# Kernel optimization log

Measured on AMD Instinct MI355X. Metric: run time of the kernel, lower is better.

Reference implementation:

```python
import jax, jax.numpy as jnp
import numpy as np

B, C, H, W = 4, 128, 128, 128
G, K = 4, 3
P = K * K
STRIDE, PAD, DIL = 1, 1, 1
OFFSET_SCALE = 1.0


def setup_inputs() -> dict:
    key = jax.random.key(0)
    k1, k2, k3, k4 = jax.random.split(key, 4)
    inp = jax.random.normal(k1, (B, C, H, W), jnp.float32)
    # offset / mask linear params (zero-init in source; small random here for a
    # nontrivial sampling pattern -- same math, different param values)
    W_off = jax.random.normal(k2, (C, G * P * 2), jnp.float32) * 0.01
    b_off = jax.random.normal(k3, (G * P * 2,), jnp.float32) * 0.5
    W_mask = jax.random.normal(k4, (C, G * P), jnp.float32) * 0.02
    b_mask = jnp.zeros((G * P,), jnp.float32)
    return {"inp": inp, "W_off": W_off, "b_off": b_off, "W_mask": W_mask, "b_mask": b_mask}


def _dcnv3_core(x, offset, mask):
    # x: (b,h,w,c)  offset: (b,h,w,G*P*2)  mask: (b,h,w,G*P)
    b, h, w, c = x.shape
    gc = c // G
    xp = jnp.pad(x, ((0, 0), (PAD, PAD), (PAD, PAD), (0, 0)))
    H_in, W_in = h + 2 * PAD, w + 2 * PAD
    H_out = (H_in - (DIL * (K - 1) + 1)) // STRIDE + 1
    W_out = (W_in - (DIL * (K - 1) + 1)) // STRIDE + 1
    Q = H_out * W_out

    # reference points, normalized to padded size (matches _get_reference_points)
    base = (DIL * (K - 1)) // 2 + 0.5
    ref_y = (base + jnp.arange(H_out, dtype=jnp.float32) * STRIDE) / H_in
    ref_x = (base + jnp.arange(W_out, dtype=jnp.float32) * STRIDE) / W_in
    ref = jnp.stack(jnp.broadcast_arrays(ref_x[None, :], ref_y[:, None]), -1)  # (Ho,Wo,2) as (x,y)

    # dilation grid (matches _generate_dilation_grids; torch meshgrid flatten is x-major)
    off0 = -((DIL * (K - 1)) // 2)
    ks = off0 + jnp.arange(K, dtype=jnp.float32) * DIL
    gx = jnp.repeat(ks, K) / W_in  # (P,)
    gy = jnp.tile(ks, K) / H_in
    grid = jnp.stack([gx, gy], -1)  # (P,2), identical for every group

    norm = jnp.array([W_in, H_in], jnp.float32)
    loc = (ref[None, :, :, None, None, :]
           + grid[None, None, None, None, :, :] * OFFSET_SCALE
           + offset.reshape(b, H_out, W_out, G, P, 2) * (OFFSET_SCALE / norm))  # (b,Ho,Wo,G,P,2)

    # grid_sample(bilinear, zeros, align_corners=False): pixel = loc*size - 0.5
    px = loc[..., 0] * W_in - 0.5
    py = loc[..., 1] * H_in - 0.5
    x0 = jnp.floor(px); y0 = jnp.floor(py)
    tx = px - x0; ty = py - y0
    x0i = x0.astype(jnp.int32); y0i = y0.astype(jnp.int32)

    xg = xp.reshape(b, H_in * W_in, G, gc)

    def corner(ix, iy, wgt):
        valid = (ix >= 0) & (ix < W_in) & (iy >= 0) & (iy < H_in)
        lin = jnp.clip(iy, 0, H_in - 1) * W_in + jnp.clip(ix, 0, W_in - 1)
        idx = lin.reshape(b, Q, G, P).transpose(0, 1, 3, 2).reshape(b, Q * P, G)
        g = jnp.take_along_axis(xg, idx[..., None], axis=1)  # (b,Q*P,G,gc)
        wv = jnp.where(valid, wgt, 0.0).reshape(b, Q, G, P).transpose(0, 1, 3, 2).reshape(b, Q * P, G, 1)
        return g * wv

    val = (corner(x0i, y0i, (1 - tx) * (1 - ty))
           + corner(x0i + 1, y0i, tx * (1 - ty))
           + corner(x0i, y0i + 1, (1 - tx) * ty)
           + corner(x0i + 1, y0i + 1, tx * ty))  # (b,Q*P,G,gc)

    m = mask.reshape(b, Q, G, P).transpose(0, 1, 3, 2).reshape(b, Q, P, G, 1)
    out = (val.reshape(b, Q, P, G, gc) * m).sum(axis=2)  # (b,Q,G,gc)
    return out.reshape(b, H_out, W_out, G * gc)


def reference(inp, W_off, b_off, W_mask, b_mask):
    b, c, h, w = inp.shape
    x = inp.reshape(b, h, w, c)  # torch .view reinterpretation (faithful to source)
    offset = x @ W_off + b_off  # (b,h,w,G*P*2)
    mask = jax.nn.softmax((x @ W_mask + b_mask).reshape(b, h, w, G, P), axis=-1).reshape(b, h, w, G * P)
    out = _dcnv3_core(x, offset, mask)  # (b,h,w,c)
    return out.reshape(b, c, h, w)
```

## Files before the change

kernel.cpp:

```cpp
#include <hip/hip_runtime.h>


#define NPIX 65536

typedef unsigned int uint;
typedef unsigned short ushort;
typedef __attribute__((ext_vector_type(8))) short short8v;
typedef __attribute__((ext_vector_type(4))) float f32x4;

__device__ __forceinline__ ushort f2bf(float f) {
  uint u = __float_as_uint(f);
  u += 0x7FFFu + ((u >> 16) & 1u);
  return (ushort)(u >> 16);
}
__device__ __forceinline__ uint pkbf(float lo, float hi) {
  return (uint)f2bf(lo) | ((uint)f2bf(hi) << 16);
}
__device__ __forceinline__ float bflo(uint d) { return __uint_as_float(d << 16); }
__device__ __forceinline__ float bfhi(uint d) { return __uint_as_float(d & 0xFFFF0000u); }

union U8 { uint u[4]; short8v v; };

__global__ __launch_bounds__(256) void dcn_lin_mfma(
    const float* __restrict__ x, const float* __restrict__ Woff,
    const float* __restrict__ boff, const float* __restrict__ Wmask,
    const float* __restrict__ bmask, float* __restrict__ ws,
    ushort* __restrict__ x16) {
  __shared__ uint wt[112 * 68];
  __shared__ float bias_lds[112];
  const int pbase = blockIdx.x << 6;
  const int t = threadIdx.x;

  {
    int n = t, row = 0;
    bool act = true;
    if (t >= 224) act = false;
    else if (t >= 112) { n = t - 112; row = 1; }
    if (act) {
      for (int kp = row; kp < 64; kp += 2) {
        const int k = kp << 1;
        float w0, w1;
        if (n < 72) {
          w0 = Woff[k * 72 + n];        w1 = Woff[k * 72 + 72 + n];
        } else if (n < 108) {
          w0 = Wmask[k * 36 + n - 72];  w1 = Wmask[k * 36 + 36 + n - 72];
        } else {
          w0 = 0.f; w1 = 0.f;
        }
        wt[n * 68 + kp] = pkbf(w0, w1);
      }
    }
    if (t < 112)
      bias_lds[t] = (t < 72) ? boff[t] : (t < 108 ? bmask[t - 72] : 0.f);
  }

  if (x16) {
    const int pix2 = pbase + (t >> 2);
    const int quad = t & 3;
    const float* xp = x + (size_t)pix2 * 128 + (quad << 5);
    const int bb = pix2 >> 14, yx = pix2 & 16383;
    ushort* dst = x16 + ((((size_t)((quad << 2) | bb) << 14) | yx) << 5);
#pragma unroll
    for (int ck = 0; ck < 2; ++ck) {
      const float4 a = *(const float4*)(xp + ck * 16);
      const float4 b4 = *(const float4*)(xp + ck * 16 + 4);
      const float4 c4 = *(const float4*)(xp + ck * 16 + 8);
      const float4 d4 = *(const float4*)(xp + ck * 16 + 12);
      uint4 s0, s1;
      s0.x = pkbf(a.x, a.y);   s0.y = pkbf(a.z, a.w);
      s0.z = pkbf(b4.x, b4.y); s0.w = pkbf(b4.z, b4.w);
      s1.x = pkbf(c4.x, c4.y); s1.y = pkbf(c4.z, c4.w);
      s1.z = pkbf(d4.x, d4.y); s1.w = pkbf(d4.z, d4.w);
      *(uint4*)(dst + ck * 16) = s0;
      *(uint4*)(dst + ck * 16 + 8) = s1;
    }
  }
  __syncthreads();

  const int wv = t >> 6;
  const int lane = t & 63;
  const int lrow = lane & 15;
  const int lhi = lane >> 4;
  const int pixrow = pbase + (wv << 4) + lrow;

  U8 afr[4];
#pragma unroll
  for (int kt = 0; kt < 4; ++kt) {
    const float* ax = x + (size_t)pixrow * 128 + (kt << 5) + (lhi << 3);
    const float4 xa = *(const float4*)ax;
    const float4 xb4 = *(const float4*)(ax + 4);
    afr[kt].u[0] = pkbf(xa.x, xa.y);   afr[kt].u[1] = pkbf(xa.z, xa.w);
    afr[kt].u[2] = pkbf(xb4.x, xb4.y); afr[kt].u[3] = pkbf(xb4.z, xb4.w);
  }

  f32x4 acc[7];
#pragma unroll
  for (int nt = 0; nt < 7; ++nt) {
    const float bv = bias_lds[(nt << 4) + lrow];
    f32x4 a4 = {bv, bv, bv, bv};
#pragma unroll
    for (int kt = 0; kt < 4; ++kt) {
      U8 bfr;
      const uint4 bw =
          *(const uint4*)(wt + ((nt << 4) + lrow) * 68 + (kt << 4) + (lhi << 2));
      bfr.u[0] = bw.x; bfr.u[1] = bw.y; bfr.u[2] = bw.z; bfr.u[3] = bw.w;
      a4 = __builtin_amdgcn_mfma_f32_16x16x32_bf16(afr[kt].v, bfr.v, a4, 0, 0, 0);
    }
    acc[nt] = a4;
  }

  const int rowb = pbase + (wv << 4) + (lhi << 2);
#pragma unroll
  for (int nt = 0; nt < 7; ++nt) {
    const int n = (nt << 4) + lrow;
    if (n < 108) *(f32x4*)(ws + (size_t)n * NPIX + rowb) = acc[nt];
  }
}

__global__ __launch_bounds__(256) void dcn_samp(
    const ushort* __restrict__ x16, const float* __restrict__ ws,
    float* __restrict__ out) {
  const int g = blockIdx.x & 3;
  const int pg = threadIdx.x >> 2;
  const int sub = threadIdx.x & 3;
  const int q = ((blockIdx.x >> 2) << 6) | pg;
  const int b = q >> 14;
  const int h = (q >> 7) & 127;
  const int w = q & 127;
  const float* wsq = ws + q;
  const ushort* xg = x16 + (((size_t)((g << 2) | b) << 14) << 5) + (sub << 3);

  float mk9[9];
  {
    float mx = -1e30f;
#pragma unroll
    for (int p = 0; p < 9; ++p) {
      mk9[p] = wsq[(size_t)(72 + g * 9 + p) * NPIX];
      mx = fmaxf(mx, mk9[p]);
    }
    float s = 0.f;
#pragma unroll
    for (int p = 0; p < 9; ++p) {
      mk9[p] = __expf(mk9[p] - mx);
      s += mk9[p];
    }
    const float sinv = 1.0f / s;
#pragma unroll
    for (int p = 0; p < 9; ++p) mk9[p] *= sinv;
  }

  float a0 = 0.f, a1 = 0.f, a2 = 0.f, a3 = 0.f;
  float a4 = 0.f, a5 = 0.f, a6 = 0.f, a7 = 0.f;

#pragma unroll
  for (int p = 0; p < 9; ++p) {
    const float offx = wsq[(size_t)(g * 18 + 2 * p) * NPIX];
    const float offy = wsq[(size_t)(g * 18 + 2 * p + 1) * NPIX];
    const float mk = mk9[p];
    const float px = (float)(w + p / 3) + offx;
    const float py = (float)(h + p % 3) + offy;
    const float fx = floorf(px), fy = floorf(py);
    const float tx = px - fx, ty = py - fy;
    const int x0 = (int)fx - 1, y0 = (int)fy - 1;
    const int x1 = x0 + 1, y1 = y0 + 1;
    const float ax0 = ((unsigned)x0 < 128u) ? (1.f - tx) : 0.f;
    const float ax1 = ((unsigned)x1 < 128u) ? tx : 0.f;
    const float ay0 = ((unsigned)y0 < 128u) ? (mk * (1.f - ty)) : 0.f;
    const float ay1 = ((unsigned)y1 < 128u) ? (mk * ty) : 0.f;
    const float w00 = ax0 * ay0, w10 = ax1 * ay0;
    const float w01 = ax0 * ay1, w11 = ax1 * ay1;
    const int cx0 = min(max(x0, 0), 127), cy0 = min(max(y0, 0), 127);
    const int cx1 = min(max(x1, 0), 127), cy1 = min(max(y1, 0), 127);
    const int o00 = ((cy0 << 7) | cx0) << 5;
    const int o10 = ((cy0 << 7) | cx1) << 5;
    const int o01 = ((cy1 << 7) | cx0) << 5;
    const int o11 = ((cy1 << 7) | cx1) << 5;
    const uint4 d00 = *(const uint4*)(xg + o00);
    const uint4 d10 = *(const uint4*)(xg + o10);
    const uint4 d01 = *(const uint4*)(xg + o01);
    const uint4 d11 = *(const uint4*)(xg + o11);
    a0 = fmaf(w00, bflo(d00.x), fmaf(w10, bflo(d10.x),
         fmaf(w01, bflo(d01.x), fmaf(w11, bflo(d11.x), a0))));
    a1 = fmaf(w00, bfhi(d00.x), fmaf(w10, bfhi(d10.x),
         fmaf(w01, bfhi(d01.x), fmaf(w11, bfhi(d11.x), a1))));
    a2 = fmaf(w00, bflo(d00.y), fmaf(w10, bflo(d10.y),
         fmaf(w01, bflo(d01.y), fmaf(w11, bflo(d11.y), a2))));
    a3 = fmaf(w00, bfhi(d00.y), fmaf(w10, bfhi(d10.y),
         fmaf(w01, bfhi(d01.y), fmaf(w11, bfhi(d11.y), a3))));
    a4 = fmaf(w00, bflo(d00.z), fmaf(w10, bflo(d10.z),
         fmaf(w01, bflo(d01.z), fmaf(w11, bflo(d11.z), a4))));
    a5 = fmaf(w00, bfhi(d00.z), fmaf(w10, bfhi(d10.z),
         fmaf(w01, bfhi(d01.z), fmaf(w11, bfhi(d11.z), a5))));
    a6 = fmaf(w00, bflo(d00.w), fmaf(w10, bflo(d10.w),
         fmaf(w01, bflo(d01.w), fmaf(w11, bflo(d11.w), a6))));
    a7 = fmaf(w00, bfhi(d00.w), fmaf(w10, bfhi(d10.w),
         fmaf(w01, bfhi(d01.w), fmaf(w11, bfhi(d11.w), a7))));
  }

  float* op = out + (size_t)q * 128 + (g << 5) + (sub << 3);
  float4 oa, ob;
  oa.x = a0; oa.y = a1; oa.z = a2; oa.w = a3;
  ob.x = a4; ob.y = a5; ob.z = a6; ob.w = a7;
  *(float4*)op = oa;
  *(float4*)(op + 4) = ob;
}

__global__ __launch_bounds__(256) void dcn_lin(
    const float* __restrict__ x, const float* __restrict__ Woff,
    const float* __restrict__ boff, const float* __restrict__ Wmask,
    const float* __restrict__ bmask, float* __restrict__ ws) {
  const int jg = blockIdx.x >> 8;
  const int pix = ((blockIdx.x & 255) << 8) | threadIdx.x;
  const float* W;
  const float* bias;
  int ldw, obase;
  if (jg == 0) {
    W = Woff; bias = boff; ldw = 72; obase = 0;
  } else if (jg == 1) {
    W = Woff + 36; bias = boff + 36; ldw = 72; obase = 36;
  } else {
    W = Wmask; bias = bmask; ldw = 36; obase = 72;
  }
  float acc[36];
#pragma unroll
  for (int j = 0; j < 36; ++j) acc[j] = bias[j];
  const float* xp = x + (size_t)pix * 128;
  for (int c0 = 0; c0 < 128; c0 += 8) {
    float xr[8];
    *(float4*)(xr) = *(const float4*)(xp + c0);
    *(float4*)(xr + 4) = *(const float4*)(xp + c0 + 4);
#pragma unroll
    for (int cc = 0; cc < 8; ++cc) {
      const float xc = xr[cc];
      const float* wr = W + (size_t)(c0 + cc) * ldw;
#pragma unroll
      for (int j = 0; j < 36; ++j) acc[j] = fmaf(xc, wr[j], acc[j]);
    }
  }
  if (jg == 2) {
#pragma unroll
    for (int g = 0; g < 4; ++g) {
      float mx = acc[g * 9];
#pragma unroll
      for (int p = 1; p < 9; ++p) mx = fmaxf(mx, acc[g * 9 + p]);
      float s = 0.f;
#pragma unroll
      for (int p = 0; p < 9; ++p) {
        acc[g * 9 + p] = __expf(acc[g * 9 + p] - mx);
        s += acc[g * 9 + p];
      }
      const float sinv = 1.0f / s;
#pragma unroll
      for (int p = 0; p < 9; ++p) acc[g * 9 + p] *= sinv;
    }
  }
#pragma unroll
  for (int j = 0; j < 36; ++j) ws[(size_t)(obase + j) * NPIX + pix] = acc[j];
}

__global__ __launch_bounds__(256) void dcn_samp_f32(
    const float* __restrict__ x, const float* __restrict__ ws,
    float* __restrict__ out) {
  const int q = (blockIdx.x << 4) | (threadIdx.x >> 4);
  const int sub = threadIdx.x & 15;
  const int c = sub << 3;
  const int g = sub >> 2;
  const int b = q >> 14;
  const int h = (q >> 7) & 127;
  const int w = q & 127;
  const float* xb = x + ((size_t)b << 21) + c;
  const float* wsq = ws + q;
  float a0 = 0.f, a1 = 0.f, a2 = 0.f, a3 = 0.f;
  float a4 = 0.f, a5 = 0.f, a6 = 0.f, a7 = 0.f;
#pragma unroll
  for (int p = 0; p < 9; ++p) {
    const float offx = wsq[(size_t)(g * 18 + p * 2) * NPIX];
    const float offy = wsq[(size_t)(g * 18 + p * 2 + 1) * NPIX];
    const float mk = wsq[(size_t)(72 + g * 9 + p) * NPIX];
    const float px = (float)(w + p / 3) + offx;
    const float py = (float)(h + p % 3) + offy;
    const float fx = floorf(px), fy = floorf(py);
    const float tx = px - fx, ty = py - fy;
    const int x0 = (int)fx - 1, y0 = (int)fy - 1;
    const int x1 = x0 + 1, y1 = y0 + 1;
    const float ax0 = ((unsigned)x0 < 128u) ? (1.f - tx) : 0.f;
    const float ax1 = ((unsigned)x1 < 128u) ? tx : 0.f;
    const float ay0 = ((unsigned)y0 < 128u) ? (mk * (1.f - ty)) : 0.f;
    const float ay1 = ((unsigned)y1 < 128u) ? (mk * ty) : 0.f;
    const float w00 = ax0 * ay0, w10 = ax1 * ay0;
    const float w01 = ax0 * ay1, w11 = ax1 * ay1;
    const int cx0 = min(max(x0, 0), 127), cy0 = min(max(y0, 0), 127);
    const int cx1 = min(max(x1, 0), 127), cy1 = min(max(y1, 0), 127);
    const int o00 = (cy0 << 14) | (cx0 << 7), o10 = (cy0 << 14) | (cx1 << 7);
    const int o01 = (cy1 << 14) | (cx0 << 7), o11 = (cy1 << 14) | (cx1 << 7);
    const float4 v00a = *(const float4*)(xb + o00);
    const float4 v00b = *(const float4*)(xb + o00 + 4);
    const float4 v10a = *(const float4*)(xb + o10);
    const float4 v10b = *(const float4*)(xb + o10 + 4);
    const float4 v01a = *(const float4*)(xb + o01);
    const float4 v01b = *(const float4*)(xb + o01 + 4);
    const float4 v11a = *(const float4*)(xb + o11);
    const float4 v11b = *(const float4*)(xb + o11 + 4);
    a0 = fmaf(w00, v00a.x, fmaf(w10, v10a.x, fmaf(w01, v01a.x, fmaf(w11, v11a.x, a0))));
    a1 = fmaf(w00, v00a.y, fmaf(w10, v10a.y, fmaf(w01, v01a.y, fmaf(w11, v11a.y, a1))));
    a2 = fmaf(w00, v00a.z, fmaf(w10, v10a.z, fmaf(w01, v01a.z, fmaf(w11, v11a.z, a2))));
    a3 = fmaf(w00, v00a.w, fmaf(w10, v10a.w, fmaf(w01, v01a.w, fmaf(w11, v11a.w, a3))));
    a4 = fmaf(w00, v00b.x, fmaf(w10, v10b.x, fmaf(w01, v01b.x, fmaf(w11, v11b.x, a4))));
    a5 = fmaf(w00, v00b.y, fmaf(w10, v10b.y, fmaf(w01, v01b.y, fmaf(w11, v11b.y, a5))));
    a6 = fmaf(w00, v00b.z, fmaf(w10, v10b.z, fmaf(w01, v01b.z, fmaf(w11, v11b.z, a6))));
    a7 = fmaf(w00, v00b.w, fmaf(w10, v10b.w, fmaf(w01, v01b.w, fmaf(w11, v11b.w, a7))));
  }
  float4 oa, ob;
  oa.x = a0; oa.y = a1; oa.z = a2; oa.w = a3;
  ob.x = a4; ob.y = a5; ob.z = a6; ob.w = a7;
  float* op = out + (size_t)q * 128 + c;
  *(float4*)op = oa;
  *(float4*)(op + 4) = ob;
}

__global__ __launch_bounds__(128) void dcn_fused(
    const float* __restrict__ x, const float* __restrict__ Woff,
    const float* __restrict__ boff, const float* __restrict__ Wmask,
    const float* __restrict__ bmask, float* __restrict__ out) {
  __shared__ float xs[128];
  __shared__ float res[108];
  __shared__ float msk[36];
  const int q = blockIdx.x;
  const int t = threadIdx.x;
  const int b = q >> 14, h = (q >> 7) & 127, w = q & 127;
  xs[t] = x[(size_t)q * 128 + t];
  __syncthreads();
  if (t < 108) {
    float a;
    const float* W;
    int ld;
    if (t < 72) {
      a = boff[t]; W = Woff + t; ld = 72;
    } else {
      a = bmask[t - 72]; W = Wmask + (t - 72); ld = 36;
    }
    for (int cc = 0; cc < 128; ++cc) a = fmaf(xs[cc], W[(size_t)cc * ld], a);
    res[t] = a;
  }
  __syncthreads();
  if (t < 4) {
    float mx = -1e30f;
    for (int p = 0; p < 9; ++p) mx = fmaxf(mx, res[72 + t * 9 + p]);
    float s = 0.f;
    float e[9];
    for (int p = 0; p < 9; ++p) {
      e[p] = __expf(res[72 + t * 9 + p] - mx);
      s += e[p];
    }
    for (int p = 0; p < 9; ++p) msk[t * 9 + p] = e[p] / s;
  }
  __syncthreads();
  const int g = t >> 5;
  const float* xb = x + ((size_t)b << 21) + t;
  float acc = 0.f;
#pragma unroll
  for (int p = 0; p < 9; ++p) {
    const float offx = res[g * 18 + p * 2];
    const float offy = res[g * 18 + p * 2 + 1];
    const float px = (float)(w + p / 3) + offx;
    const float py = (float)(h + p % 3) + offy;
    const float fx = floorf(px), fy = floorf(py);
    const float tx = px - fx, ty = py - fy;
    const int x0 = (int)fx - 1, y0 = (int)fy - 1;
    float sv = 0.f;
#define CORNER1(XI, YI, WT)                                       \
  if ((unsigned)(XI) < 128u && (unsigned)(YI) < 128u)             \
    sv = fmaf((WT), xb[((size_t)(YI) << 14) + ((size_t)(XI) << 7)], sv);
    CORNER1(x0, y0, (1.f - tx) * (1.f - ty))
    CORNER1(x0 + 1, y0, tx * (1.f - ty))
    CORNER1(x0, y0 + 1, (1.f - tx) * ty)
    CORNER1(x0 + 1, y0 + 1, tx * ty)
#undef CORNER1
    acc = fmaf(msk[g * 9 + p], sv, acc);
  }
  out[(size_t)q * 128 + t] = acc;
}

extern "C" void kernel_launch(void* const* d_in, const int* in_sizes, int n_in,
                              void* d_out, int out_size, void* d_ws,
                              size_t ws_size, hipStream_t stream) {
  const float* x = (const float*)d_in[0];
  const float* Woff = (const float*)d_in[1];
  const float* boff = (const float*)d_in[2];
  const float* Wmask = (const float*)d_in[3];
  const float* bmask = (const float*)d_in[4];
  float* out = (float*)d_out;
  const size_t need_ws = (size_t)NPIX * 108 * sizeof(float);
  const size_t need_full = need_ws + (size_t)NPIX * 128 * sizeof(ushort);
  if (ws_size >= need_full) {
    float* ws = (float*)d_ws;
    ushort* x16 = (ushort*)((char*)d_ws + need_ws);
    dcn_lin_mfma<<<1024, 256, 0, stream>>>(x, Woff, boff, Wmask, bmask, ws, x16);
    dcn_samp<<<4096, 256, 0, stream>>>(x16, ws, out);
  } else if (ws_size >= need_ws) {
    float* ws = (float*)d_ws;
    dcn_lin<<<768, 256, 0, stream>>>(x, Woff, boff, Wmask, bmask, ws);
    dcn_samp_f32<<<4096, 256, 0, stream>>>(x, ws, out);
  } else {
    dcn_fused<<<NPIX, 128, 0, stream>>>(x, Woff, boff, Wmask, bmask, out);
  }
}
```

Measured before the change: 62.74 us.

## Store offsets/mask in fp16, tile sampler spatially, batch corner loads

The linear kernel now writes the offset and mask workspace as fp16 instead of fp32, which halves that intermediate traffic. The sampler maps each block to a 4x16 spatial tile instead of a 64-pixel row strip, so neighbouring bilinear gathers share cache lines. The 9 taps are processed in groups of 3, with all corner loads issued before the FMAs to raise memory-level parallelism, and the launch bounds now ask for 4 blocks per CU. The risks are reduced precision for offsets (fp16 positions near 128 carry about 0.06 of error), more registers live at once, and a workspace layout change.

```diff
diff --git a/kernel.cpp b/kernel.cpp
--- a/kernel.cpp
+++ b/kernel.cpp
@@ -18,13 +18,23 @@
 }
 __device__ __forceinline__ float bflo(uint d) { return __uint_as_float(d << 16); }
 __device__ __forceinline__ float bfhi(uint d) { return __uint_as_float(d & 0xFFFF0000u); }
+__device__ __forceinline__ ushort f2h(float f) {
+  union { _Float16 h; ushort u; } cv;
+  cv.h = (_Float16)f;
+  return cv.u;
+}
+__device__ __forceinline__ float h2f(ushort u) {
+  union { ushort u; _Float16 h; } cv;
+  cv.u = u;
+  return (float)cv.h;
+}
 
 union U8 { uint u[4]; short8v v; };
 
 __global__ __launch_bounds__(256) void dcn_lin_mfma(
     const float* __restrict__ x, const float* __restrict__ Woff,
     const float* __restrict__ boff, const float* __restrict__ Wmask,
-    const float* __restrict__ bmask, float* __restrict__ ws,
+    const float* __restrict__ bmask, ushort* __restrict__ ws16,
     ushort* __restrict__ x16) {
   __shared__ uint wt[112 * 68];
   __shared__ float bias_lds[112];
@@ -113,29 +123,39 @@
 #pragma unroll
   for (int nt = 0; nt < 7; ++nt) {
     const int n = (nt << 4) + lrow;
-    if (n < 108) *(f32x4*)(ws + (size_t)n * NPIX + rowb) = acc[nt];
-  }
-}
-
-__global__ __launch_bounds__(256) void dcn_samp(
-    const ushort* __restrict__ x16, const float* __restrict__ ws,
+    if (n < 108) {
+      ushort4 hv;
+      hv.x = f2h(acc[nt].x);
+      hv.y = f2h(acc[nt].y);
+      hv.z = f2h(acc[nt].z);
+      hv.w = f2h(acc[nt].w);
+      *(ushort4*)(ws16 + (size_t)n * NPIX + rowb) = hv;
+    }
+  }
+}
+
+__global__ __launch_bounds__(256, 4) void dcn_samp(
+    const ushort* __restrict__ x16, const ushort* __restrict__ ws16,
     float* __restrict__ out) {
   const int g = blockIdx.x & 3;
+  const int tile = blockIdx.x >> 2;
+  const int b = tile >> 8;
+  const int ty = (tile >> 3) & 31;
+  const int tx = tile & 7;
   const int pg = threadIdx.x >> 2;
   const int sub = threadIdx.x & 3;
-  const int q = ((blockIdx.x >> 2) << 6) | pg;
-  const int b = q >> 14;
-  const int h = (q >> 7) & 127;
-  const int w = q & 127;
-  const float* wsq = ws + q;
-  const ushort* xg = x16 + (((size_t)((g << 2) | b) << 14) << 5) + (sub << 3);
+  const int yy = pg >> 4, xx = pg & 15;
+  const int h = (ty << 2) | yy, w = (tx << 4) | xx;
+  const int q = (b << 14) | (h << 7) | w;
+  const ushort* wsq = ws16 + q;
+  const ushort* xg = x16 + (((size_t)((g << 2) | b)) << 19) + (sub << 3);
 
   float mk9[9];
   {
     float mx = -1e30f;
 #pragma unroll
     for (int p = 0; p < 9; ++p) {
-      mk9[p] = wsq[(size_t)(72 + g * 9 + p) * NPIX];
+      mk9[p] = h2f(wsq[(size_t)(72 + g * 9 + p) * NPIX]);
       mx = fmaxf(mx, mk9[p]);
     }
     float s = 0.f;
@@ -153,48 +173,60 @@
   float a4 = 0.f, a5 = 0.f, a6 = 0.f, a7 = 0.f;
 
 #pragma unroll
-  for (int p = 0; p < 9; ++p) {
-    const float offx = wsq[(size_t)(g * 18 + 2 * p) * NPIX];
-    const float offy = wsq[(size_t)(g * 18 + 2 * p + 1) * NPIX];
-    const float mk = mk9[p];
-    const float px = (float)(w + p / 3) + offx;
-    const float py = (float)(h + p % 3) + offy;
-    const float fx = floorf(px), fy = floorf(py);
-    const float tx = px - fx, ty = py - fy;
-    const int x0 = (int)fx - 1, y0 = (int)fy - 1;
-    const int x1 = x0 + 1, y1 = y0 + 1;
-    const float ax0 = ((unsigned)x0 < 128u) ? (1.f - tx) : 0.f;
-    const float ax1 = ((unsigned)x1 < 128u) ? tx : 0.f;
-    const float ay0 = ((unsigned)y0 < 128u) ? (mk * (1.f - ty)) : 0.f;
-    const float ay1 = ((unsigned)y1 < 128u) ? (mk * ty) : 0.f;
-    const float w00 = ax0 * ay0, w10 = ax1 * ay0;
-    const float w01 = ax0 * ay1, w11 = ax1 * ay1;
-    const int cx0 = min(max(x0, 0), 127), cy0 = min(max(y0, 0), 127);
-    const int cx1 = min(max(x1, 0), 127), cy1 = min(max(y1, 0), 127);
-    const int o00 = ((cy0 << 7) | cx0) << 5;
-    const int o10 = ((cy0 << 7) | cx1) << 5;
-    const int o01 = ((cy1 << 7) | cx0) << 5;
-    const int o11 = ((cy1 << 7) | cx1) << 5;
-    const uint4 d00 = *(const uint4*)(xg + o00);
-    const uint4 d10 = *(const uint4*)(xg + o10);
-    const uint4 d01 = *(const uint4*)(xg + o01);
-    const uint4 d11 = *(const uint4*)(xg + o11);
-    a0 = fmaf(w00, bflo(d00.x), fmaf(w10, bflo(d10.x),
-         fmaf(w01, bflo(d01.x), fmaf(w11, bflo(d11.x), a0))));
-    a1 = fmaf(w00, bfhi(d00.x), fmaf(w10, bfhi(d10.x),
-         fmaf(w01, bfhi(d01.x), fmaf(w11, bfhi(d11.x), a1))));
-    a2 = fmaf(w00, bflo(d00.y), fmaf(w10, bflo(d10.y),
-         fmaf(w01, bflo(d01.y), fmaf(w11, bflo(d11.y), a2))));
-    a3 = fmaf(w00, bfhi(d00.y), fmaf(w10, bfhi(d10.y),
-         fmaf(w01, bfhi(d01.y), fmaf(w11, bfhi(d11.y), a3))));
-    a4 = fmaf(w00, bflo(d00.z), fmaf(w10, bflo(d10.z),
-         fmaf(w01, bflo(d01.z), fmaf(w11, bflo(d11.z), a4))));
-    a5 = fmaf(w00, bfhi(d00.z), fmaf(w10, bfhi(d10.z),
-         fmaf(w01, bfhi(d01.z), fmaf(w11, bfhi(d11.z), a5))));
-    a6 = fmaf(w00, bflo(d00.w), fmaf(w10, bflo(d10.w),
-         fmaf(w01, bflo(d01.w), fmaf(w11, bflo(d11.w), a6))));
-    a7 = fmaf(w00, bfhi(d00.w), fmaf(w10, bfhi(d10.w),
-         fmaf(w01, bfhi(d01.w), fmaf(w11, bfhi(d11.w), a7))));
+  for (int bt = 0; bt < 3; ++bt) {
+    float w00[3], w10[3], w01[3], w11[3];
+    int o00[3], o10[3], o01[3], o11[3];
+#pragma unroll
+    for (int i = 0; i < 3; ++i) {
+      const int p = bt * 3 + i;
+      const float offx = h2f(wsq[(size_t)(g * 18 + 2 * p) * NPIX]);
+      const float offy = h2f(wsq[(size_t)(g * 18 + 2 * p + 1) * NPIX]);
+      const float px = (float)(w + p / 3) + offx;
+      const float py = (float)(h + p % 3) + offy;
+      const float fx = floorf(px), fy = floorf(py);
+      const float txf = px - fx, tyf = py - fy;
+      const int x0 = (int)fx - 1, y0 = (int)fy - 1;
+      const int x1 = x0 + 1, y1 = y0 + 1;
+      const float ax0 = ((unsigned)x0 < 128u) ? (1.f - txf) : 0.f;
+      const float ax1 = ((unsigned)x1 < 128u) ? txf : 0.f;
+      const float ay0 = ((unsigned)y0 < 128u) ? (mk9[p] * (1.f - tyf)) : 0.f;
+      const float ay1 = ((unsigned)y1 < 128u) ? (mk9[p] * tyf) : 0.f;
+      w00[i] = ax0 * ay0; w10[i] = ax1 * ay0;
+      w01[i] = ax0 * ay1; w11[i] = ax1 * ay1;
+      const int cx0 = min(max(x0, 0), 127), cy0 = min(max(y0, 0), 127);
+      const int cx1 = min(max(x1, 0), 127), cy1 = min(max(y1, 0), 127);
+      o00[i] = ((cy0 << 7) | cx0) << 5;
+      o10[i] = ((cy0 << 7) | cx1) << 5;
+      o01[i] = ((cy1 << 7) | cx0) << 5;
+      o11[i] = ((cy1 << 7) | cx1) << 5;
+    }
+    uint4 d00[3], d10[3], d01[3], d11[3];
+#pragma unroll
+    for (int i = 0; i < 3; ++i) {
+      d00[i] = *(const uint4*)(xg + o00[i]);
+      d10[i] = *(const uint4*)(xg + o10[i]);
+      d01[i] = *(const uint4*)(xg + o01[i]);
+      d11[i] = *(const uint4*)(xg + o11[i]);
+    }
+#pragma unroll
+    for (int i = 0; i < 3; ++i) {
+      a0 = fmaf(w00[i], bflo(d00[i].x), fmaf(w10[i], bflo(d10[i].x),
+           fmaf(w01[i], bflo(d01[i].x), fmaf(w11[i], bflo(d11[i].x), a0))));
+      a1 = fmaf(w00[i], bfhi(d00[i].x), fmaf(w10[i], bfhi(d10[i].x),
+           fmaf(w01[i], bfhi(d01[i].x), fmaf(w11[i], bfhi(d11[i].x), a1))));
+      a2 = fmaf(w00[i], bflo(d00[i].y), fmaf(w10[i], bflo(d10[i].y),
+           fmaf(w01[i], bflo(d01[i].y), fmaf(w11[i], bflo(d11[i].y), a2))));
+      a3 = fmaf(w00[i], bfhi(d00[i].y), fmaf(w10[i], bfhi(d10[i].y),
+           fmaf(w01[i], bfhi(d01[i].y), fmaf(w11[i], bfhi(d11[i].y), a3))));
+      a4 = fmaf(w00[i], bflo(d00[i].z), fmaf(w10[i], bflo(d10[i].z),
+           fmaf(w01[i], bflo(d01[i].z), fmaf(w11[i], bflo(d11[i].z), a4))));
+      a5 = fmaf(w00[i], bfhi(d00[i].z), fmaf(w10[i], bfhi(d10[i].z),
+           fmaf(w01[i], bfhi(d01[i].z), fmaf(w11[i], bfhi(d11[i].z), a5))));
+      a6 = fmaf(w00[i], bflo(d00[i].w), fmaf(w10[i], bflo(d10[i].w),
+           fmaf(w01[i], bflo(d01[i].w), fmaf(w11[i], bflo(d11[i].w), a6))));
+      a7 = fmaf(w00[i], bfhi(d00[i].w), fmaf(w10[i], bfhi(d10[i].w),
+           fmaf(w01[i], bfhi(d01[i].w), fmaf(w11[i], bfhi(d11[i].w), a7))));
+    }
   }
 
   float* op = out + (size_t)q * 128 + (g << 5) + (sub << 3);
@@ -391,12 +423,13 @@
   const float* bmask = (const float*)d_in[4];
   float* out = (float*)d_out;
   const size_t need_ws = (size_t)NPIX * 108 * sizeof(float);
-  const size_t need_full = need_ws + (size_t)NPIX * 128 * sizeof(ushort);
+  const size_t need_full = (size_t)NPIX * (128 + 108) * sizeof(ushort);
   if (ws_size >= need_full) {
-    float* ws = (float*)d_ws;
-    ushort* x16 = (ushort*)((char*)d_ws + need_ws);
-    dcn_lin_mfma<<<1024, 256, 0, stream>>>(x, Woff, boff, Wmask, bmask, ws, x16);
-    dcn_samp<<<4096, 256, 0, stream>>>(x16, ws, out);
+    ushort* x16 = (ushort*)d_ws;
+    ushort* ws16 = (ushort*)d_ws + (size_t)NPIX * 128;
+    dcn_lin_mfma<<<1024, 256, 0, stream>>>(x, Woff, boff, Wmask, bmask, ws16,
+                                           x16);
+    dcn_samp<<<4096, 256, 0, stream>>>(x16, ws16, out);
   } else if (ws_size >= need_ws) {
     float* ws = (float*)d_ws;
     dcn_lin<<<768, 256, 0, stream>>>(x, Woff, boff, Wmask, bmask, ws);
```

Measured after the change: 125.0 us. +99.2%, slower.
